# Kernel tuning notes

Hardware: AMD Instinct MI355X
Metric: run time of the kernel (lower is better)

## Reference

```python
import jax, jax.numpy as jnp
import numpy as np

B, T, D, R = 16, 4096, 512, 256

# Buffers (match torch: linspace(0,T-1,R).long() truncates toward zero)
_LANDMARKS = np.linspace(0.0, T - 1, R).astype(np.int64)
_POS = np.arange(T)[:, None]                                   # [T,1]
_MASK = (_LANDMARKS[None, :] < _POS)                           # [T,R] bool: landmark j < position i
_TDIST = np.clip((_POS.astype(np.float32) - _LANDMARKS[None, :].astype(np.float32)) / T, 0.0, None).astype(np.float32)  # [T,R]


def setup_inputs() -> dict:
    key = jax.random.key(0)
    k1, k2, k3 = jax.random.split(key, 3)
    return {
        "z": jax.random.normal(k1, (B, T, D), dtype=jnp.float32),
        "gegenbauer_weights": jax.random.normal(k2, (3,), dtype=jnp.float32),
        "temporal_alpha": jax.random.normal(k3, (1,), dtype=jnp.float32),
    }


def reference(z, gegenbauer_weights, temporal_alpha):
    dtype = z.dtype
    mask = jnp.asarray(_MASK)                       # [T,R]
    tdist = jnp.asarray(_TDIST, dtype=dtype)        # [T,R]
    lm = jnp.asarray(_LANDMARKS)                    # [R]

    # F.normalize(z, dim=-1) with eps=1e-12
    norm = jnp.linalg.norm(z, axis=-1, keepdims=True)
    Q = z / jnp.maximum(norm, 1e-12)                # [B,T,D]
    K = Q[:, lm, :]                                 # [B,R,D]
    C = jnp.einsum('btd,brd->btr', Q, K)            # [B,T,R] cosine similarity

    # Gegenbauer mixture
    alpha = jax.nn.softmax(gegenbauer_weights)
    C2 = C * C
    P1 = (1.0 + C) * 0.5
    P2 = (3.0 * C2 - 1.0) * 0.5
    P3 = (5.0 * C2 * C - 3.0 * C) * 0.5
    Phi = alpha[0] * P1 + alpha[1] * P2 + alpha[2] * P3

    # Causal mask
    Phi = Phi * mask.astype(dtype)[None, :, :]

    # Temporal decay
    a_td = jax.nn.softplus(temporal_alpha[0])
    Phi = Phi * jnp.exp(-a_td * tdist)[None, :, :]

    # Row-sum normalization
    row_sum = jnp.maximum(Phi.sum(axis=-1, keepdims=True), 1e-6)
    Phi = Phi / row_sum

    # Append constant-ones feature -> [B,T,R+1]
    ones = jnp.ones((Phi.shape[0], Phi.shape[1], 1), dtype=dtype)
    return jnp.concatenate([Phi, ones], axis=-1)
```

## Files before the change

kernel.cpp:

```cpp
#include <hip/hip_runtime.h>
#include <hip/hip_bf16.h>
#include <math.h>

#define B_DIM 16
#define T_DIM 4096
#define D_DIM 512
#define R_DIM 256

#define TM 64
#define BK 32
#define NKCH 16
#define CHUNK 32768

typedef __bf16 bf16x8 __attribute__((ext_vector_type(8)));
typedef float floatx4 __attribute__((ext_vector_type(4)));

__device__ __forceinline__ int landmark_of(int r) {
    if (r >= 255) return 4095;
    const double step = 4095.0 / 255.0;
    return (int)((double)r * step);
}

__device__ __forceinline__ void split_bf16(float x, __bf16& h, __bf16& l) {
    h = (__bf16)x;
    l = (__bf16)(x - (float)h);
}

__device__ __forceinline__ void async_copy16(const void* g, void* l) {
    __builtin_amdgcn_global_load_lds(
        (const __attribute__((address_space(1))) unsigned int*)g,
        (__attribute__((address_space(3))) unsigned int*)l, 16, 0, 0);
}

__global__ void nystrom_prep_kernel(const float* __restrict__ z, char* __restrict__ blob) {
    int blk = blockIdx.x;
    int b = blk >> 8;
    int r = blk & 255;
    int lane = threadIdx.x;
    int lm = landmark_of(r);
    const float* src = z + ((size_t)b * T_DIM + lm) * D_DIM + lane * 8;
    float4 v0 = ((const float4*)src)[0];
    float4 v1 = ((const float4*)src)[1];
    float ss = v0.x*v0.x + v0.y*v0.y + v0.z*v0.z + v0.w*v0.w
             + v1.x*v1.x + v1.y*v1.y + v1.z*v1.z + v1.w*v1.w;
    #pragma unroll
    for (int off = 1; off < 64; off <<= 1) ss += __shfl_xor(ss, off, 64);
    float inv = 1.0f / fmaxf(sqrtf(ss), 1e-12f);
    float qv[8] = {v0.x*inv, v0.y*inv, v0.z*inv, v0.w*inv,
                   v1.x*inv, v1.y*inv, v1.z*inv, v1.w*inv};
    bf16x8 oh, ol;
    #pragma unroll
    for (int j = 0; j < 8; j++) { __bf16 h, l; split_bf16(qv[j], h, l); oh[j] = h; ol[j] = l; }
    int kc = lane >> 2, g = lane & 3;
    char* dst = blob + ((size_t)(b * NKCH + kc)) * CHUNK + r * 64 + 16 * ((g + r) & 3);
    *(bf16x8*)dst = oh;
    *(bf16x8*)(dst + 16384) = ol;
}

__global__ __launch_bounds__(256, 3)
void nystrom_main_kernel(const float* __restrict__ z, const char* __restrict__ blob,
                         const float* __restrict__ gw, const float* __restrict__ ta,
                         float* __restrict__ out) {
    __shared__ __attribute__((aligned(16))) char smem[40960];
    __bf16* Bs = (__bf16*)smem;
    char*   Asb = smem + 32768;
    float* rnorm_s = (float*)(smem + 32768);
    float* rspart  = (float*)(smem + 32768 + 256);

    const int tid  = threadIdx.x;
    const int b    = blockIdx.y;
    const int t0   = blockIdx.x * TM;
    const int lane = tid & 63;
    const int wv   = tid >> 6;
    const int q    = lane >> 4;
    const int ln   = lane & 15;

    float g0 = gw[0], g1 = gw[1], g2 = gw[2];
    float gm = fmaxf(g0, fmaxf(g1, g2));
    float e0 = expf(g0 - gm), e1 = expf(g1 - gm), e2 = expf(g2 - gm);
    float esum = e0 + e1 + e2;
    float al0 = e0 / esum, al1 = e1 / esum, al2 = e2 / esum;
    float ax = ta[0];
    float a_td = (ax > 20.f) ? ax : log1pf(expf(ax));

    const int arow = tid >> 2, ag = tid & 3;
    const float* zsrc = z + ((size_t)b * T_DIM + t0 + arow) * D_DIM + ag * 8;
    char* awh = Asb + arow * 64 + 16 * ((ag + arow) & 3);
    char* awl = awh + 4096;

    const char* bsrc0 = blob + (size_t)(b * NKCH) * CHUNK + wv * 8192 + lane * 16;
    char* bdst0 = smem + wv * 8192;

    floatx4 acc[4][4];
    #pragma unroll
    for (int i = 0; i < 4; i++)
        #pragma unroll
        for (int j = 0; j < 4; j++) acc[i][j] = (floatx4){0.f, 0.f, 0.f, 0.f};
    float ssq = 0.0f;

    float4 pa0 = *(const float4*)(zsrc);
    float4 pa1 = *(const float4*)(zsrc + 4);

    #pragma unroll 1
    for (int kt = 0; kt < NKCH; kt++) {
        {
            float av[8] = {pa0.x, pa0.y, pa0.z, pa0.w, pa1.x, pa1.y, pa1.z, pa1.w};
            bf16x8 h8, l8;
            #pragma unroll
            for (int j = 0; j < 8; j++) {
                ssq += av[j] * av[j];
                __bf16 h, l; split_bf16(av[j], h, l); h8[j] = h; l8[j] = l;
            }
            *(bf16x8*)awh = h8;
            *(bf16x8*)awl = l8;
        }
        {
            const char* bs = bsrc0 + (size_t)kt * CHUNK;
            #pragma unroll
            for (int i = 0; i < 8; i++)
                async_copy16(bs + i * 1024, bdst0 + i * 1024);
        }
        __syncthreads();

        if (kt + 1 < NKCH) {
            const float* zp = zsrc + (kt + 1) * BK;
            pa0 = *(const float4*)(zp);
            pa1 = *(const float4*)(zp + 4);
        }

        {
            const int rot = 16 * ((q + ln) & 3);
            bf16x8 bh[4], bl[4];
            #pragma unroll
            for (int ni = 0; ni < 4; ni++) {
                const char* p = (const char*)Bs + (wv * 64 + ni * 16 + ln) * 64 + rot;
                bh[ni] = *(const bf16x8*)p;
                bl[ni] = *(const bf16x8*)(p + 16384);
            }
            #pragma unroll
            for (int mi = 0; mi < 4; mi++) {
                const char* pa = Asb + (mi * 16 + ln) * 64 + rot;
                bf16x8 ah = *(const bf16x8*)pa;
                bf16x8 al = *(const bf16x8*)(pa + 4096);
                #pragma unroll
                for (int ni = 0; ni < 4; ni++) {
                    acc[mi][ni] = __builtin_amdgcn_mfma_f32_16x16x32_bf16(ah, bh[ni], acc[mi][ni], 0, 0, 0);
                    acc[mi][ni] = __builtin_amdgcn_mfma_f32_16x16x32_bf16(ah, bl[ni], acc[mi][ni], 0, 0, 0);
                    acc[mi][ni] = __builtin_amdgcn_mfma_f32_16x16x32_bf16(al, bh[ni], acc[mi][ni], 0, 0, 0);
                }
            }
        }
        __syncthreads();
    }

    ssq += __shfl_xor(ssq, 1, 64);
    ssq += __shfl_xor(ssq, 2, 64);
    if (ag == 0) rnorm_s[arow] = 1.0f / fmaxf(sqrtf(ssq), 1e-12f);
    __syncthreads();

    int   lm_r[4];
    float elm_r[4];
    #pragma unroll
    for (int ni = 0; ni < 4; ni++) {
        int r = wv * 64 + ni * 16 + ln;
        lm_r[ni]  = landmark_of(r);
        elm_r[ni] = expf(a_td * (float)lm_r[ni] * (1.0f / 4096.0f));
    }

    #pragma unroll
    for (int mi = 0; mi < 4; mi++) {
        #pragma unroll
        for (int reg = 0; reg < 4; reg++) {
            const int row = mi * 16 + q * 4 + reg;
            const int t = t0 + row;
            const float rn = rnorm_s[row];
            const float e_t = expf(-a_td * (float)t * (1.0f / 4096.0f));
            float s = 0.f;
            #pragma unroll
            for (int ni = 0; ni < 4; ni++) {
                float phi = 0.f;
                if (lm_r[ni] < t) {
                    float c  = acc[mi][ni][reg] * rn;
                    float c2 = c * c;
                    float P1 = 0.5f * (1.f + c);
                    float P2 = 0.5f * (3.f * c2 - 1.f);
                    float P3 = 0.5f * (5.f * c2 * c - 3.f * c);
                    float p  = al0 * P1 + al1 * P2 + al2 * P3;
                    phi = p * e_t * elm_r[ni];
                }
                acc[mi][ni][reg] = phi;
                s += phi;
            }
            s += __shfl_xor(s, 1, 64);
            s += __shfl_xor(s, 2, 64);
            s += __shfl_xor(s, 4, 64);
            s += __shfl_xor(s, 8, 64);
            if (ln == 0) rspart[wv * 64 + row] = s;
        }
    }
    __syncthreads();

    float* ob = out + ((size_t)b * T_DIM + t0) * 257;
    #pragma unroll
    for (int mi = 0; mi < 4; mi++) {
        #pragma unroll
        for (int reg = 0; reg < 4; reg++) {
            const int row = mi * 16 + q * 4 + reg;
            float rs = rspart[row] + rspart[64 + row] + rspart[128 + row] + rspart[192 + row];
            float inv = 1.0f / fmaxf(rs, 1e-6f);
            #pragma unroll
            for (int ni = 0; ni < 4; ni++) {
                ob[(size_t)row * 257 + wv * 64 + ni * 16 + ln] = acc[mi][ni][reg] * inv;
            }
        }
    }
    if (tid < TM) ob[(size_t)tid * 257 + 256] = 1.0f;
}

extern "C" void kernel_launch(void* const* d_in, const int* in_sizes, int n_in,
                              void* d_out, int out_size, void* d_ws, size_t ws_size,
                              hipStream_t stream) {
    const float* z  = (const float*)d_in[0];
    const float* gw = (const float*)d_in[1];
    const float* ta = (const float*)d_in[2];
    float* out = (float*)d_out;
    char* blob = (char*)d_ws;

    nystrom_prep_kernel<<<dim3(B_DIM * R_DIM), 64, 0, stream>>>(z, blob);
    nystrom_main_kernel<<<dim3(T_DIM / TM, B_DIM), 256, 0, stream>>>(z, blob, gw, ta, out);
}
```

Baseline: 270.2 us.

## Double-buffer A and B LDS tiles and change the swizzle to cut bank conflicts

The main loop now uses two LDS buffers for both the landmark (B) tiles and the converted z (A) tiles. The async copy of the next-but-one chunk is issued right after a barrier, so global-to-LDS transfers overlap MFMA work and the loop needs only one barrier per K-chunk. The LDS swizzle also changes to mix bits from both row&3 and (row>>2)&3, to reduce bank conflicts on the 16-byte fragment reads. In exchange, LDS use doubles to 80 KB and the launch bound drops from 3 to 2 blocks per CU, which lowers occupancy.

After: 257.2 us. 1.05x faster.

```diff
diff --git a/kernel.cpp b/kernel.cpp
--- a/kernel.cpp
+++ b/kernel.cpp
@@ -8,7 +8,6 @@
 #define R_DIM 256
 
 #define TM 64
-#define BK 32
 #define NKCH 16
 #define CHUNK 32768
 
@@ -24,6 +23,10 @@
 __device__ __forceinline__ void split_bf16(float x, __bf16& h, __bf16& l) {
     h = (__bf16)x;
     l = (__bf16)(x - (float)h);
+}
+
+__device__ __forceinline__ int swz(int row, int g) {
+    return 16 * ((g + (row & 3) + ((row >> 2) & 3)) & 3);
 }
 
 __device__ __forceinline__ void async_copy16(const void* g, void* l) {
@@ -52,20 +55,53 @@
     #pragma unroll
     for (int j = 0; j < 8; j++) { __bf16 h, l; split_bf16(qv[j], h, l); oh[j] = h; ol[j] = l; }
     int kc = lane >> 2, g = lane & 3;
-    char* dst = blob + ((size_t)(b * NKCH + kc)) * CHUNK + r * 64 + 16 * ((g + r) & 3);
+    char* dst = blob + ((size_t)(b * NKCH + kc)) * CHUNK + r * 64 + swz(r, g);
     *(bf16x8*)dst = oh;
     *(bf16x8*)(dst + 16384) = ol;
 }
 
-__global__ __launch_bounds__(256, 3)
+__device__ __forceinline__ void stage_a(float4 v0, float4 v1, char* abuf, int awoff, float& ssq) {
+    float av[8] = {v0.x, v0.y, v0.z, v0.w, v1.x, v1.y, v1.z, v1.w};
+    bf16x8 h8, l8;
+    #pragma unroll
+    for (int j = 0; j < 8; j++) {
+        ssq += av[j] * av[j];
+        __bf16 h, l; split_bf16(av[j], h, l); h8[j] = h; l8[j] = l;
+    }
+    *(bf16x8*)(abuf + awoff) = h8;
+    *(bf16x8*)(abuf + awoff + 4096) = l8;
+}
+
+__device__ __forceinline__ void mfma_phase(const char* bB, const char* bA,
+                                           int wv, int ln, int rot, floatx4 (&acc)[4][4]) {
+    bf16x8 bh[4], bl[4];
+    #pragma unroll
+    for (int ni = 0; ni < 4; ni++) {
+        const char* p = bB + (wv * 64 + ni * 16 + ln) * 64 + rot;
+        bh[ni] = *(const bf16x8*)p;
+        bl[ni] = *(const bf16x8*)(p + 16384);
+    }
+    #pragma unroll
+    for (int mi = 0; mi < 4; mi++) {
+        const char* pA = bA + (mi * 16 + ln) * 64 + rot;
+        bf16x8 ah = *(const bf16x8*)pA;
+        bf16x8 al = *(const bf16x8*)(pA + 4096);
+        #pragma unroll
+        for (int ni = 0; ni < 4; ni++) {
+            acc[mi][ni] = __builtin_amdgcn_mfma_f32_16x16x32_bf16(ah, bh[ni], acc[mi][ni], 0, 0, 0);
+            acc[mi][ni] = __builtin_amdgcn_mfma_f32_16x16x32_bf16(ah, bl[ni], acc[mi][ni], 0, 0, 0);
+            acc[mi][ni] = __builtin_amdgcn_mfma_f32_16x16x32_bf16(al, bh[ni], acc[mi][ni], 0, 0, 0);
+        }
+    }
+}
+
+__global__ __launch_bounds__(256, 2)
 void nystrom_main_kernel(const float* __restrict__ z, const char* __restrict__ blob,
                          const float* __restrict__ gw, const float* __restrict__ ta,
                          float* __restrict__ out) {
-    __shared__ __attribute__((aligned(16))) char smem[40960];
-    __bf16* Bs = (__bf16*)smem;
-    char*   Asb = smem + 32768;
-    float* rnorm_s = (float*)(smem + 32768);
-    float* rspart  = (float*)(smem + 32768 + 256);
+    __shared__ __attribute__((aligned(16))) char smem[81920];
+    float* rnorm_s = (float*)(smem + 65536);
+    float* rspart  = (float*)(smem + 65536 + 256);
 
     const int tid  = threadIdx.x;
     const int b    = blockIdx.y;
@@ -85,11 +121,12 @@
 
     const int arow = tid >> 2, ag = tid & 3;
     const float* zsrc = z + ((size_t)b * T_DIM + t0 + arow) * D_DIM + ag * 8;
-    char* awh = Asb + arow * 64 + 16 * ((ag + arow) & 3);
-    char* awl = awh + 4096;
-
-    const char* bsrc0 = blob + (size_t)(b * NKCH) * CHUNK + wv * 8192 + lane * 16;
-    char* bdst0 = smem + wv * 8192;
+    const int awoff = arow * 64 + swz(arow, ag);
+
+    const char* bsrc = blob + (size_t)(b * NKCH) * CHUNK + wv * 8192 + lane * 16;
+    const int bdoff = wv * 8192;
+
+    const int rot = swz(ln, q);
 
     floatx4 acc[4][4];
     #pragma unroll
@@ -98,59 +135,47 @@
         for (int j = 0; j < 4; j++) acc[i][j] = (floatx4){0.f, 0.f, 0.f, 0.f};
     float ssq = 0.0f;
 
-    float4 pa0 = *(const float4*)(zsrc);
-    float4 pa1 = *(const float4*)(zsrc + 4);
+    #pragma unroll
+    for (int i = 0; i < 8; i++) async_copy16(bsrc + i * 1024, smem + bdoff + i * 1024);
+    float4 pa0a = *(const float4*)(zsrc);
+    float4 pa0b = *(const float4*)(zsrc + 4);
+    float4 pa1a = *(const float4*)(zsrc + 32);
+    float4 pa1b = *(const float4*)(zsrc + 36);
+    stage_a(pa0a, pa0b, smem + 65536, awoff, ssq);
+    __syncthreads();
+    #pragma unroll
+    for (int i = 0; i < 8; i++) async_copy16(bsrc + CHUNK + i * 1024, smem + 32768 + bdoff + i * 1024);
 
     #pragma unroll 1
-    for (int kt = 0; kt < NKCH; kt++) {
-        {
-            float av[8] = {pa0.x, pa0.y, pa0.z, pa0.w, pa1.x, pa1.y, pa1.z, pa1.w};
-            bf16x8 h8, l8;
-            #pragma unroll
-            for (int j = 0; j < 8; j++) {
-                ssq += av[j] * av[j];
-                __bf16 h, l; split_bf16(av[j], h, l); h8[j] = h; l8[j] = l;
-            }
-            *(bf16x8*)awh = h8;
-            *(bf16x8*)awl = l8;
-        }
-        {
-            const char* bs = bsrc0 + (size_t)kt * CHUNK;
-            #pragma unroll
-            for (int i = 0; i < 8; i++)
-                async_copy16(bs + i * 1024, bdst0 + i * 1024);
-        }
+    for (int kt2 = 0; kt2 < 8; kt2++) {
+        const int kt = kt2 * 2;
+        const bool more = (kt2 < 7);
+        stage_a(pa1a, pa1b, smem + 65536 + 8192, awoff, ssq);
+        if (more) {
+            const float* zp = zsrc + (kt + 2) * 32;
+            pa0a = *(const float4*)(zp);
+            pa0b = *(const float4*)(zp + 4);
+        }
+        mfma_phase(smem, smem + 65536, wv, ln, rot, acc);
         __syncthreads();
-
-        if (kt + 1 < NKCH) {
-            const float* zp = zsrc + (kt + 1) * BK;
-            pa0 = *(const float4*)(zp);
-            pa1 = *(const float4*)(zp + 4);
-        }
-
-        {
-            const int rot = 16 * ((q + ln) & 3);
-            bf16x8 bh[4], bl[4];
-            #pragma unroll
-            for (int ni = 0; ni < 4; ni++) {
-                const char* p = (const char*)Bs + (wv * 64 + ni * 16 + ln) * 64 + rot;
-                bh[ni] = *(const bf16x8*)p;
-                bl[ni] = *(const bf16x8*)(p + 16384);
-            }
-            #pragma unroll
-            for (int mi = 0; mi < 4; mi++) {
-                const char* pa = Asb + (mi * 16 + ln) * 64 + rot;
-                bf16x8 ah = *(const bf16x8*)pa;
-                bf16x8 al = *(const bf16x8*)(pa + 4096);
-                #pragma unroll
-                for (int ni = 0; ni < 4; ni++) {
-                    acc[mi][ni] = __builtin_amdgcn_mfma_f32_16x16x32_bf16(ah, bh[ni], acc[mi][ni], 0, 0, 0);
-                    acc[mi][ni] = __builtin_amdgcn_mfma_f32_16x16x32_bf16(ah, bl[ni], acc[mi][ni], 0, 0, 0);
-                    acc[mi][ni] = __builtin_amdgcn_mfma_f32_16x16x32_bf16(al, bh[ni], acc[mi][ni], 0, 0, 0);
-                }
-            }
-        }
+        if (more) {
+            const char* s2 = bsrc + (size_t)(kt + 2) * CHUNK;
+            #pragma unroll
+            for (int i = 0; i < 8; i++) async_copy16(s2 + i * 1024, smem + bdoff + i * 1024);
+        }
+        if (more) stage_a(pa0a, pa0b, smem + 65536, awoff, ssq);
+        if (more) {
+            const float* zp = zsrc + (kt + 3) * 32;
+            pa1a = *(const float4*)(zp);
+            pa1b = *(const float4*)(zp + 4);
+        }
+        mfma_phase(smem + 32768, smem + 65536 + 8192, wv, ln, rot, acc);
         __syncthreads();
+        if (more) {
+            const char* s3 = bsrc + (size_t)(kt + 3) * CHUNK;
+            #pragma unroll
+            for (int i = 0; i < 8; i++) async_copy16(s3 + i * 1024, smem + 32768 + bdoff + i * 1024);
+        }
     }
 
     ssq += __shfl_xor(ssq, 1, 64);
```
